# Kernel optimization log

Hardware: AMD Instinct MI355X
Metric: run time of the kernel (lower is better)

Reference implementation:

```python
import jax, jax.numpy as jnp
from jax import lax
import numpy as np

H = 10  # GRU hidden size
MAX_ACTION = 1.0


def _gru_final(x, w_ih, w_hh, b_ih, b_hh, reverse):
    """Run a single-direction GRU over x [B,T,1]; return final hidden [B,H].

    PyTorch GRU gate math:
      r = sigmoid(W_ir x + b_ir + W_hr h + b_hr)
      z = sigmoid(W_iz x + b_iz + W_hz h + b_hz)
      n = tanh(W_in x + b_in + r * (W_hn h + b_hn))
      h' = (1 - z) * n + z * h
    """
    # Precompute input contributions for all timesteps: [B,T,3H]
    gx = jnp.einsum('bti,gi->btg', x, w_ih) + b_ih
    if reverse:
        gx = gx[:, ::-1]

    def step(h, g_t):
        gh = h @ w_hh.T + b_hh
        xr, xz, xn = jnp.split(g_t, 3, axis=-1)
        hr, hz, hn = jnp.split(gh, 3, axis=-1)
        r = jax.nn.sigmoid(xr + hr)
        z = jax.nn.sigmoid(xz + hz)
        n = jnp.tanh(xn + r * hn)
        return (1.0 - z) * n + z * h, None

    h0 = jnp.zeros((x.shape[0], H), x.dtype)
    hT, _ = lax.scan(step, h0, jnp.swapaxes(gx, 0, 1))  # scan over T
    return hT


def _bigru_feats(x, wf_ih, wf_hh, bf_ih, bf_hh, wb_ih, wb_hh, bb_ih, bb_hh):
    # Equivalent to cat(out[:, -1, :H], out[:, 0, H:]) for a bi-GRU: the
    # final hidden of each direction.
    hf = _gru_final(x, wf_ih, wf_hh, bf_ih, bf_hh, reverse=False)
    hb = _gru_final(x, wb_ih, wb_hh, bb_ih, bb_hh, reverse=True)
    return jnp.concatenate([hf, hb], axis=-1)  # [B, 2H]


def setup_inputs() -> dict:
    key = jax.random.key(0)
    ks = jax.random.split(key, 24)
    B, action_dim = 2097152, 2
    s = 0.3

    def n(k, shape):
        return jax.random.normal(k, shape, dtype=jnp.float32) * s

    inp = {'state': jax.random.normal(ks[0], (B, 10), dtype=jnp.float32)}
    i = 1
    for g in ('1', '2'):
        for d in ('f', 'b'):
            inp[f'w_ih_{g}{d}'] = n(ks[i], (3 * H, 1)); i += 1
            inp[f'w_hh_{g}{d}'] = n(ks[i], (3 * H, H)); i += 1
            inp[f'b_ih_{g}{d}'] = n(ks[i], (3 * H,)); i += 1
            inp[f'b_hh_{g}{d}'] = n(ks[i], (3 * H,)); i += 1
    inp['l1_w'] = n(ks[i], (20, 40)); i += 1
    inp['l1_b'] = n(ks[i], (20,)); i += 1
    inp['l2_w'] = n(ks[i], (action_dim, 20)); i += 1
    inp['l2_b'] = n(ks[i], (action_dim,))
    return inp


def reference(state,
              w_ih_1f, w_hh_1f, b_ih_1f, b_hh_1f,
              w_ih_1b, w_hh_1b, b_ih_1b, b_hh_1b,
              w_ih_2f, w_hh_2f, b_ih_2f, b_hh_2f,
              w_ih_2b, w_hh_2b, b_ih_2b, b_hh_2b,
              l1_w, l1_b, l2_w, l2_b):
    x1 = state[:, :5, None]  # [B,5,1]
    x2 = state[:, 5:, None]  # [B,5,1]
    cat1 = _bigru_feats(x1, w_ih_1f, w_hh_1f, b_ih_1f, b_hh_1f,
                        w_ih_1b, w_hh_1b, b_ih_1b, b_hh_1b)
    cat2 = _bigru_feats(x2, w_ih_2f, w_hh_2f, b_ih_2f, b_hh_2f,
                        w_ih_2b, w_hh_2b, b_ih_2b, b_hh_2b)
    feats = jnp.concatenate([cat1, cat2], axis=-1)  # [B,40]
    a = jax.nn.selu(feats @ l1_w.T + l1_b)
    a = a @ l2_w.T + l2_b
    return jnp.clip(a, -MAX_ACTION, MAX_ACTION)
```

## Files before the change

kernel.cpp:

```cpp
#include <hip/hip_runtime.h>


#define NH 10

typedef float f32x2 __attribute__((ext_vector_type(2)));
struct __align__(16) q2 { f32x2 lo, hi; };

__device__ __forceinline__ float frcp(float x) { return __builtin_amdgcn_rcpf(x); }
__device__ __forceinline__ float fexp2(float x) { return __builtin_amdgcn_exp2f(x); }
__device__ __forceinline__ float fexp(float x) { return __expf(x); }

__device__ __forceinline__ f32x2 pk_fma_lo(f32x2 a, f32x2 b, f32x2 c) {
    f32x2 d;
    asm("v_pk_fma_f32 %0, %1, %2, %3 op_sel_hi:[1,0,1]" : "=v"(d) : "v"(a), "v"(b), "v"(c));
    return d;
}
__device__ __forceinline__ f32x2 pk_fma_hi(f32x2 a, f32x2 b, f32x2 c) {
    f32x2 d;
    asm("v_pk_fma_f32 %0, %1, %2, %3 op_sel:[0,1,0] op_sel_hi:[1,1,1]" : "=v"(d) : "v"(a), "v"(b), "v"(c));
    return d;
}
__device__ __forceinline__ f32x2 pk_fma_bh_cl(f32x2 a, f32x2 b, f32x2 c) {
    f32x2 d;
    asm("v_pk_fma_f32 %0, %1, %2, %3 op_sel:[0,1,0] op_sel_hi:[1,1,0]" : "=v"(d) : "v"(a), "v"(b), "v"(c));
    return d;
}
__device__ __forceinline__ f32x2 pk_fma_bl_cl(f32x2 a, f32x2 b, f32x2 c) {
    f32x2 d;
    asm("v_pk_fma_f32 %0, %1, %2, %3 op_sel_hi:[1,0,0]" : "=v"(d) : "v"(a), "v"(b), "v"(c));
    return d;
}
__device__ __forceinline__ f32x2 pk_fma(f32x2 a, f32x2 b, f32x2 c) {
    f32x2 d;
    asm("v_pk_fma_f32 %0, %1, %2, %3" : "=v"(d) : "v"(a), "v"(b), "v"(c));
    return d;
}

#define PDOT9(acc, hh, q1, q2_, q3)                  \
    acc = pk_fma_hi(hh[1], (q1).lo, acc);            \
    acc = pk_fma_lo(hh[2], (q1).hi, acc);            \
    acc = pk_fma_hi(hh[3], (q1).hi, acc);            \
    acc = pk_fma_lo(hh[4], (q2_).lo, acc);           \
    acc = pk_fma_hi(hh[5], (q2_).lo, acc);           \
    acc = pk_fma_lo(hh[6], (q2_).hi, acc);           \
    acc = pk_fma_hi(hh[7], (q2_).hi, acc);           \
    acc = pk_fma_lo(hh[8], (q3).lo, acc);            \
    acc = pk_fma_hi(hh[9], (q3).lo, acc);

#define LDQ(p) (*(const q2*)(p))

__global__ __launch_bounds__(256) void actor_kernel(
    const float* __restrict__ state,
    const float* __restrict__ wih0, const float* __restrict__ whh0,
    const float* __restrict__ bih0, const float* __restrict__ bhh0,
    const float* __restrict__ wih1, const float* __restrict__ whh1,
    const float* __restrict__ bih1, const float* __restrict__ bhh1,
    const float* __restrict__ wih2, const float* __restrict__ whh2,
    const float* __restrict__ bih2, const float* __restrict__ bhh2,
    const float* __restrict__ wih3, const float* __restrict__ whh3,
    const float* __restrict__ bih3, const float* __restrict__ bhh3,
    const float* __restrict__ l1w, const float* __restrict__ l1b,
    const float* __restrict__ l2w, const float* __restrict__ l2b,
    float* __restrict__ out, int Btot)
{
    __shared__ __align__(16) float s_w[4][360];
    __shared__ __align__(8) f32x2 s_bihn2[4][10];
    __shared__ __align__(16) float s_l1w[20][48];
    __shared__ float s_l1b[20];
    __shared__ __align__(8) f32x2 s_l2w2[2][20];
    __shared__ float s_l2b[2];

    const int tid = threadIdx.x;
    const float NL2E = -1.4426950408889634f;
    const float P2L2E = 2.8853900817779268f;

#define STAGE_DIR(d, wihP, whhP, bihP, bhhP)                                   \
    for (int i = tid; i < 360; i += 256) {                                     \
        int g = i / 12, s = i % 12;                                            \
        float sc = (g < 20) ? NL2E : P2L2E;                                    \
        float v;                                                               \
        if (s < 10)       v = whhP[g * 10 + s] * sc;                           \
        else if (s == 10) v = ((g < 20) ? (bihP[g] + bhhP[g]) : bhhP[g]) * sc; \
        else              v = wihP[g] * sc;                                    \
        s_w[d][g * 12 + s] = v;                                                \
    }                                                                          \
    for (int i = tid; i < 10; i += 256) {                                      \
        float v = bihP[20 + i] * P2L2E;                                        \
        s_bihn2[d][i] = (f32x2){v, v};                                         \
    }

    STAGE_DIR(0, wih0, whh0, bih0, bhh0)
    STAGE_DIR(1, wih1, whh1, bih1, bhh1)
    STAGE_DIR(2, wih2, whh2, bih2, bhh2)
    STAGE_DIR(3, wih3, whh3, bih3, bhh3)
#undef STAGE_DIR
    for (int i = tid; i < 960; i += 256) {
        int o = i / 48, c = i % 48, dd = c / 12, jj = c % 12;
        s_l1w[o][c] = (jj < 10) ? l1w[o * 40 + dd * 10 + jj] : 0.0f;
    }
    for (int i = tid; i < 20; i += 256) s_l1b[i] = l1b[i];
    for (int i = tid; i < 40; i += 256) {
        float v = l2w[i];
        s_l2w2[i / 20][i % 20] = (f32x2){v, v};
    }
    for (int i = tid; i < 2; i += 256) s_l2b[i] = l2b[i];
    __syncthreads();

    const int q = tid >> 2;
    const int d = tid & 3;
    long long rA = (long long)blockIdx.x * 128 + 2 * q;
    long long rB = rA + 1;
    const bool vA = (rA < Btot), vB = (rB < Btot);
    if (rA >= Btot) rA = Btot - 1;
    if (rB >= Btot) rB = Btot - 1;

    f32x2 xq2[5];
    {
        const float* pA = state + rA * 10 + ((d & 2) ? 5 : 0);
        const float* pB = state + rB * 10 + ((d & 2) ? 5 : 0);
        const int rev = d & 1;
#pragma unroll
        for (int i = 0; i < 5; ++i) {
            int k = rev ? (4 - i) : i;
            xq2[i] = (f32x2){pA[k], pB[k]};
        }
    }

    const float* wb0 = &s_w[d][0];
    const f32x2* bn2 = &s_bihn2[d][0];

    f32x2 h2[NH];
#pragma unroll
    for (int j = 0; j < NH; ++j) h2[j] = (f32x2){0.0f, 0.0f};

    unsigned hoff = 0;
#pragma unroll 1
    for (int tt = 0; tt < 5; ++tt) {
        asm volatile("" : "+v"(hoff));
        const float* wb = wb0 + hoff;
        const f32x2 xt2 = xq2[0];
#pragma unroll
        for (int i = 0; i < 4; ++i) xq2[i] = xq2[i + 1];

        f32x2 hn2[NH];
#pragma unroll
        for (int j = 0; j < NH; ++j) {
            const float* rp = wb + j * 12;
            const float* zp = wb + (j + 10) * 12;
            const float* np = wb + (j + 20) * 12;
            q2 rq0 = LDQ(rp), rq1 = LDQ(rp + 4), rq2 = LDQ(rp + 8);
            q2 zq0 = LDQ(zp), zq1 = LDQ(zp + 4), zq2 = LDQ(zp + 8);
            q2 nq0 = LDQ(np), nq1 = LDQ(np + 4), nq2 = LDQ(np + 8);

            f32x2 ar = pk_fma_bh_cl(xt2, rq2.hi, rq2.hi);
            ar = pk_fma_lo(h2[0], rq0.lo, ar);
            PDOT9(ar, h2, rq0, rq1, rq2)
            f32x2 az = pk_fma_bh_cl(xt2, zq2.hi, zq2.hi);
            az = pk_fma_lo(h2[0], zq0.lo, az);
            PDOT9(az, h2, zq0, zq1, zq2)
            f32x2 an = pk_fma_bl_cl(h2[0], nq0.lo, nq2.hi);
            PDOT9(an, h2, nq0, nq1, nq2)
            f32x2 xn = pk_fma_bh_cl(xt2, nq2.hi, bn2[j]);

            f32x2 rr, zz, e, nn;
            rr.x = frcp(1.0f + fexp2(ar.x)); rr.y = frcp(1.0f + fexp2(ar.y));
            zz.x = frcp(1.0f + fexp2(az.x)); zz.y = frcp(1.0f + fexp2(az.y));
            e.x = fexp2(fmaf(rr.x, an.x, xn.x)); e.y = fexp2(fmaf(rr.y, an.y, xn.y));
            nn.x = fmaf(-2.0f, frcp(e.x + 1.0f), 1.0f);
            nn.y = fmaf(-2.0f, frcp(e.y + 1.0f), 1.0f);
            f32x2 t = h2[j] - nn;
            hn2[j] = pk_fma(zz, t, nn);
        }
#pragma unroll
        for (int j = 0; j < NH; ++j) h2[j] = hn2[j];
    }

    f32x2 a1[20];
#pragma unroll
    for (int o = 0; o < 20; ++o) {
        const float* lw = &s_l1w[o][0] + d * 12;
        q2 c0 = LDQ(lw), c1 = LDQ(lw + 4), c2 = LDQ(lw + 8);
        f32x2 s = pk_fma_bl_cl(h2[0], c0.lo, c2.hi);
        PDOT9(s, h2, c0, c1, c2)
        a1[o] = s;
    }
#pragma unroll
    for (int o = 0; o < 20; ++o) {
        f32x2 v = a1[o];
        v.x += __shfl_xor(v.x, 1, 64);
        v.x += __shfl_xor(v.x, 2, 64);
        v.y += __shfl_xor(v.y, 1, 64);
        v.y += __shfl_xor(v.y, 2, 64);
        a1[o] = v;
    }

    const float SC = 1.0507009873554805f;
    const float AL = 1.6732632423543772f;
    f32x2 o0 = (f32x2){s_l2b[0], s_l2b[0]};
    f32x2 o1 = (f32x2){s_l2b[1], s_l2b[1]};
#pragma unroll
    for (int o = 0; o < 20; ++o) {
        f32x2 s;
        s.x = a1[o].x + s_l1b[o];
        s.y = a1[o].y + s_l1b[o];
        s.x = (s.x > 0.0f) ? SC * s.x : SC * AL * (fexp(s.x) - 1.0f);
        s.y = (s.y > 0.0f) ? SC * s.y : SC * AL * (fexp(s.y) - 1.0f);
        o0 = pk_fma_lo(s, s_l2w2[0][o], o0);
        o1 = pk_fma_lo(s, s_l2w2[1][o], o1);
    }
    o0.x = fminf(1.0f, fmaxf(-1.0f, o0.x));
    o0.y = fminf(1.0f, fmaxf(-1.0f, o0.y));
    o1.x = fminf(1.0f, fmaxf(-1.0f, o1.x));
    o1.y = fminf(1.0f, fmaxf(-1.0f, o1.y));

    if (d == 0) {
        if (vA && vB) {
            *reinterpret_cast<float4*>(out + rA * 2) = make_float4(o0.x, o1.x, o0.y, o1.y);
        } else {
            if (vA) reinterpret_cast<float2*>(out)[rA] = make_float2(o0.x, o1.x);
            if (vB) reinterpret_cast<float2*>(out)[rB] = make_float2(o0.y, o1.y);
        }
    }
}

extern "C" void kernel_launch(void* const* d_in, const int* in_sizes, int n_in,
                              void* d_out, int out_size, void* d_ws, size_t ws_size,
                              hipStream_t stream) {
    const float* state = (const float*)d_in[0];
    const int B = in_sizes[0] / 10;
    const int grid = (B + 127) / 128;

    actor_kernel<<<grid, 256, 0, stream>>>(
        state,
        (const float*)d_in[1],  (const float*)d_in[2],  (const float*)d_in[3],  (const float*)d_in[4],
        (const float*)d_in[5],  (const float*)d_in[6],  (const float*)d_in[7],  (const float*)d_in[8],
        (const float*)d_in[9],  (const float*)d_in[10], (const float*)d_in[11], (const float*)d_in[12],
        (const float*)d_in[13], (const float*)d_in[14], (const float*)d_in[15], (const float*)d_in[16],
        (const float*)d_in[17], (const float*)d_in[18], (const float*)d_in[19], (const float*)d_in[20],
        (float*)d_out, B);
}
```

Before: 555.5 us.

## Process four batch rows per thread to amortize LDS weight loads

Each thread now handles two packed row pairs (four rows) instead of one pair, so every weight quad loaded from LDS in the GRU recurrence and the first linear layer serves twice as many FMAs. The grid is halved to match, and the L1 reduction, SELU and L2 are fused into one loop, which drops the a1[20] array. This cuts LDS traffic per row and adds independent work per thread for ILP. The cost is roughly double the register pressure for hidden state and accumulators, which may lower occupancy or cause spills.

```diff
diff --git a/kernel.cpp b/kernel.cpp
--- a/kernel.cpp
+++ b/kernel.cpp
@@ -108,41 +108,47 @@
 
     const int q = tid >> 2;
     const int d = tid & 3;
-    long long rA = (long long)blockIdx.x * 128 + 2 * q;
-    long long rB = rA + 1;
-    const bool vA = (rA < Btot), vB = (rB < Btot);
-    if (rA >= Btot) rA = Btot - 1;
-    if (rB >= Btot) rB = Btot - 1;
-
-    f32x2 xq2[5];
+    long long base = (long long)blockIdx.x * 256 + 4 * q;
+    long long r0 = base, r1 = base + 1, r2 = base + 2, r3 = base + 3;
+    const bool v01 = (r1 < Btot), v23 = (r3 < Btot);
+    if (r0 >= Btot) r0 = Btot - 1;
+    if (r1 >= Btot) r1 = Btot - 1;
+    if (r2 >= Btot) r2 = Btot - 1;
+    if (r3 >= Btot) r3 = Btot - 1;
+
+    f32x2 xqp[5], xqq[5];
     {
-        const float* pA = state + rA * 10 + ((d & 2) ? 5 : 0);
-        const float* pB = state + rB * 10 + ((d & 2) ? 5 : 0);
+        const int off = (d & 2) ? 5 : 0;
+        const float* p0 = state + r0 * 10 + off;
+        const float* p1 = state + r1 * 10 + off;
+        const float* p2 = state + r2 * 10 + off;
+        const float* p3 = state + r3 * 10 + off;
         const int rev = d & 1;
 #pragma unroll
         for (int i = 0; i < 5; ++i) {
             int k = rev ? (4 - i) : i;
-            xq2[i] = (f32x2){pA[k], pB[k]};
+            xqp[i] = (f32x2){p0[k], p1[k]};
+            xqq[i] = (f32x2){p2[k], p3[k]};
         }
     }
 
     const float* wb0 = &s_w[d][0];
     const f32x2* bn2 = &s_bihn2[d][0];
 
-    f32x2 h2[NH];
-#pragma unroll
-    for (int j = 0; j < NH; ++j) h2[j] = (f32x2){0.0f, 0.0f};
+    f32x2 hp[NH], hq[NH];
+#pragma unroll
+    for (int j = 0; j < NH; ++j) { hp[j] = (f32x2){0.0f, 0.0f}; hq[j] = (f32x2){0.0f, 0.0f}; }
 
     unsigned hoff = 0;
 #pragma unroll 1
     for (int tt = 0; tt < 5; ++tt) {
         asm volatile("" : "+v"(hoff));
         const float* wb = wb0 + hoff;
-        const f32x2 xt2 = xq2[0];
-#pragma unroll
-        for (int i = 0; i < 4; ++i) xq2[i] = xq2[i + 1];
-
-        f32x2 hn2[NH];
+        const f32x2 xtp = xqp[0], xtq = xqq[0];
+#pragma unroll
+        for (int i = 0; i < 4; ++i) { xqp[i] = xqp[i + 1]; xqq[i] = xqq[i + 1]; }
+
+        f32x2 hnp[NH], hnq[NH];
 #pragma unroll
         for (int j = 0; j < NH; ++j) {
             const float* rp = wb + j * 12;
@@ -151,74 +157,87 @@
             q2 rq0 = LDQ(rp), rq1 = LDQ(rp + 4), rq2 = LDQ(rp + 8);
             q2 zq0 = LDQ(zp), zq1 = LDQ(zp + 4), zq2 = LDQ(zp + 8);
             q2 nq0 = LDQ(np), nq1 = LDQ(np + 4), nq2 = LDQ(np + 8);
-
-            f32x2 ar = pk_fma_bh_cl(xt2, rq2.hi, rq2.hi);
-            ar = pk_fma_lo(h2[0], rq0.lo, ar);
-            PDOT9(ar, h2, rq0, rq1, rq2)
-            f32x2 az = pk_fma_bh_cl(xt2, zq2.hi, zq2.hi);
-            az = pk_fma_lo(h2[0], zq0.lo, az);
-            PDOT9(az, h2, zq0, zq1, zq2)
-            f32x2 an = pk_fma_bl_cl(h2[0], nq0.lo, nq2.hi);
-            PDOT9(an, h2, nq0, nq1, nq2)
-            f32x2 xn = pk_fma_bh_cl(xt2, nq2.hi, bn2[j]);
-
-            f32x2 rr, zz, e, nn;
-            rr.x = frcp(1.0f + fexp2(ar.x)); rr.y = frcp(1.0f + fexp2(ar.y));
-            zz.x = frcp(1.0f + fexp2(az.x)); zz.y = frcp(1.0f + fexp2(az.y));
-            e.x = fexp2(fmaf(rr.x, an.x, xn.x)); e.y = fexp2(fmaf(rr.y, an.y, xn.y));
-            nn.x = fmaf(-2.0f, frcp(e.x + 1.0f), 1.0f);
-            nn.y = fmaf(-2.0f, frcp(e.y + 1.0f), 1.0f);
-            f32x2 t = h2[j] - nn;
-            hn2[j] = pk_fma(zz, t, nn);
+            const f32x2 bnj = bn2[j];
+
+            f32x2 arP = pk_fma_bh_cl(xtp, rq2.hi, rq2.hi);
+            arP = pk_fma_lo(hp[0], rq0.lo, arP);
+            PDOT9(arP, hp, rq0, rq1, rq2)
+            f32x2 azP = pk_fma_bh_cl(xtp, zq2.hi, zq2.hi);
+            azP = pk_fma_lo(hp[0], zq0.lo, azP);
+            PDOT9(azP, hp, zq0, zq1, zq2)
+            f32x2 anP = pk_fma_bl_cl(hp[0], nq0.lo, nq2.hi);
+            PDOT9(anP, hp, nq0, nq1, nq2)
+            f32x2 xnP = pk_fma_bh_cl(xtp, nq2.hi, bnj);
+
+            f32x2 arQ = pk_fma_bh_cl(xtq, rq2.hi, rq2.hi);
+            arQ = pk_fma_lo(hq[0], rq0.lo, arQ);
+            PDOT9(arQ, hq, rq0, rq1, rq2)
+            f32x2 azQ = pk_fma_bh_cl(xtq, zq2.hi, zq2.hi);
+            azQ = pk_fma_lo(hq[0], zq0.lo, azQ);
+            PDOT9(azQ, hq, zq0, zq1, zq2)
+            f32x2 anQ = pk_fma_bl_cl(hq[0], nq0.lo, nq2.hi);
+            PDOT9(anQ, hq, nq0, nq1, nq2)
+            f32x2 xnQ = pk_fma_bh_cl(xtq, nq2.hi, bnj);
+
+            f32x2 rrP, zzP, eP, nnP, rrQ, zzQ, eQ, nnQ;
+            rrP.x = frcp(1.0f + fexp2(arP.x)); rrP.y = frcp(1.0f + fexp2(arP.y));
+            zzP.x = frcp(1.0f + fexp2(azP.x)); zzP.y = frcp(1.0f + fexp2(azP.y));
+            eP.x = fexp2(fmaf(rrP.x, anP.x, xnP.x)); eP.y = fexp2(fmaf(rrP.y, anP.y, xnP.y));
+            nnP.x = fmaf(-2.0f, frcp(eP.x + 1.0f), 1.0f);
+            nnP.y = fmaf(-2.0f, frcp(eP.y + 1.0f), 1.0f);
+            rrQ.x = frcp(1.0f + fexp2(arQ.x)); rrQ.y = frcp(1.0f + fexp2(arQ.y));
+            zzQ.x = frcp(1.0f + fexp2(azQ.x)); zzQ.y = frcp(1.0f + fexp2(azQ.y));
+            eQ.x = fexp2(fmaf(rrQ.x, anQ.x, xnQ.x)); eQ.y = fexp2(fmaf(rrQ.y, anQ.y, xnQ.y));
+            nnQ.x = fmaf(-2.0f, frcp(eQ.x + 1.0f), 1.0f);
+            nnQ.y = fmaf(-2.0f, frcp(eQ.y + 1.0f), 1.0f);
+
+            hnp[j] = pk_fma(zzP, hp[j] - nnP, nnP);
+            hnq[j] = pk_fma(zzQ, hq[j] - nnQ, nnQ);
         }
 #pragma unroll
-        for (int j = 0; j < NH; ++j) h2[j] = hn2[j];
-    }
-
-    f32x2 a1[20];
+        for (int j = 0; j < NH; ++j) { hp[j] = hnp[j]; hq[j] = hnq[j]; }
+    }
+
+    const float SC = 1.0507009873554805f;
+    const float AL = 1.6732632423543772f;
+    f32x2 o0P = (f32x2){s_l2b[0], s_l2b[0]};
+    f32x2 o1P = (f32x2){s_l2b[1], s_l2b[1]};
+    f32x2 o0Q = o0P, o1Q = o1P;
 #pragma unroll
     for (int o = 0; o < 20; ++o) {
         const float* lw = &s_l1w[o][0] + d * 12;
         q2 c0 = LDQ(lw), c1 = LDQ(lw + 4), c2 = LDQ(lw + 8);
-        f32x2 s = pk_fma_bl_cl(h2[0], c0.lo, c2.hi);
-        PDOT9(s, h2, c0, c1, c2)
-        a1[o] = s;
-    }
-#pragma unroll
-    for (int o = 0; o < 20; ++o) {
-        f32x2 v = a1[o];
-        v.x += __shfl_xor(v.x, 1, 64);
-        v.x += __shfl_xor(v.x, 2, 64);
-        v.y += __shfl_xor(v.y, 1, 64);
-        v.y += __shfl_xor(v.y, 2, 64);
-        a1[o] = v;
-    }
-
-    const float SC = 1.0507009873554805f;
-    const float AL = 1.6732632423543772f;
-    f32x2 o0 = (f32x2){s_l2b[0], s_l2b[0]};
-    f32x2 o1 = (f32x2){s_l2b[1], s_l2b[1]};
-#pragma unroll
-    for (int o = 0; o < 20; ++o) {
-        f32x2 s;
-        s.x = a1[o].x + s_l1b[o];
-        s.y = a1[o].y + s_l1b[o];
-        s.x = (s.x > 0.0f) ? SC * s.x : SC * AL * (fexp(s.x) - 1.0f);
-        s.y = (s.y > 0.0f) ? SC * s.y : SC * AL * (fexp(s.y) - 1.0f);
-        o0 = pk_fma_lo(s, s_l2w2[0][o], o0);
-        o1 = pk_fma_lo(s, s_l2w2[1][o], o1);
-    }
-    o0.x = fminf(1.0f, fmaxf(-1.0f, o0.x));
-    o0.y = fminf(1.0f, fmaxf(-1.0f, o0.y));
-    o1.x = fminf(1.0f, fmaxf(-1.0f, o1.x));
-    o1.y = fminf(1.0f, fmaxf(-1.0f, o1.y));
+        f32x2 sP = pk_fma_bl_cl(hp[0], c0.lo, c2.hi);
+        PDOT9(sP, hp, c0, c1, c2)
+        f32x2 sQ = pk_fma_bl_cl(hq[0], c0.lo, c2.hi);
+        PDOT9(sQ, hq, c0, c1, c2)
+        sP.x += __shfl_xor(sP.x, 1, 64); sP.x += __shfl_xor(sP.x, 2, 64);
+        sP.y += __shfl_xor(sP.y, 1, 64); sP.y += __shfl_xor(sP.y, 2, 64);
+        sQ.x += __shfl_xor(sQ.x, 1, 64); sQ.x += __shfl_xor(sQ.x, 2, 64);
+        sQ.y += __shfl_xor(sQ.y, 1, 64); sQ.y += __shfl_xor(sQ.y, 2, 64);
+        const float b = s_l1b[o];
+        float s0 = sP.x + b, s1 = sP.y + b, s2 = sQ.x + b, s3 = sQ.y + b;
+        s0 = (s0 > 0.0f) ? SC * s0 : SC * AL * (fexp(s0) - 1.0f);
+        s1 = (s1 > 0.0f) ? SC * s1 : SC * AL * (fexp(s1) - 1.0f);
+        s2 = (s2 > 0.0f) ? SC * s2 : SC * AL * (fexp(s2) - 1.0f);
+        s3 = (s3 > 0.0f) ? SC * s3 : SC * AL * (fexp(s3) - 1.0f);
+        f32x2 suP = (f32x2){s0, s1}, suQ = (f32x2){s2, s3};
+        o0P = pk_fma(suP, s_l2w2[0][o], o0P);
+        o1P = pk_fma(suP, s_l2w2[1][o], o1P);
+        o0Q = pk_fma(suQ, s_l2w2[0][o], o0Q);
+        o1Q = pk_fma(suQ, s_l2w2[1][o], o1Q);
+    }
+    o0P.x = fminf(1.0f, fmaxf(-1.0f, o0P.x)); o0P.y = fminf(1.0f, fmaxf(-1.0f, o0P.y));
+    o1P.x = fminf(1.0f, fmaxf(-1.0f, o1P.x)); o1P.y = fminf(1.0f, fmaxf(-1.0f, o1P.y));
+    o0Q.x = fminf(1.0f, fmaxf(-1.0f, o0Q.x)); o0Q.y = fminf(1.0f, fmaxf(-1.0f, o0Q.y));
+    o1Q.x = fminf(1.0f, fmaxf(-1.0f, o1Q.x)); o1Q.y = fminf(1.0f, fmaxf(-1.0f, o1Q.y));
 
     if (d == 0) {
-        if (vA && vB) {
-            *reinterpret_cast<float4*>(out + rA * 2) = make_float4(o0.x, o1.x, o0.y, o1.y);
-        } else {
-            if (vA) reinterpret_cast<float2*>(out)[rA] = make_float2(o0.x, o1.x);
-            if (vB) reinterpret_cast<float2*>(out)[rB] = make_float2(o0.y, o1.y);
+        if (v01) *reinterpret_cast<float4*>(out + base * 2) = make_float4(o0P.x, o1P.x, o0P.y, o1P.y);
+        if (v23) *reinterpret_cast<float4*>(out + base * 2 + 4) = make_float4(o0Q.x, o1Q.x, o0Q.y, o1Q.y);
+        if (!v01 || !v23) {
+            if (r0 < Btot && !v01) reinterpret_cast<float2*>(out)[r0] = make_float2(o0P.x, o1P.x);
+            if (r2 < Btot && !v23) reinterpret_cast<float2*>(out)[r2] = make_float2(o0Q.x, o1Q.x);
         }
     }
 }
@@ -228,7 +247,7 @@
                               hipStream_t stream) {
     const float* state = (const float*)d_in[0];
     const int B = in_sizes[0] / 10;
-    const int grid = (B + 127) / 128;
+    const int grid = (B + 255) / 256;
 
     actor_kernel<<<grid, 256, 0, stream>>>(
         state,
```

Result: faster. 508.4 us (median of 2 runs) (-8.5%).
